# Performance work log

Hardware: AMD Instinct MI355X
Metric: run time of the kernel (lower is better)

The kernel has to match this reference:

```python
import jax, jax.numpy as jnp
import numpy as np

B, H, W, D = 4, 64, 64, 384
M, P = 12, 9
DH = D // M             # 32 head dim
DFF = 3 * D             # 1152 FFN hidden
N = H * W               # 4096 queries (single level)


def setup_inputs():
    key = jax.random.key(0)
    ks = jax.random.split(key, 12)
    g = lambda k, s, sc=0.02: jax.random.normal(k, s, jnp.float32) * sc
    return {
        "x": jax.random.normal(ks[0], (B, D, H, W), jnp.float32),
        "qry_masks": jnp.zeros((B, H, W), jnp.float32),
        "so_w": g(ks[1], (M * P * 2, D)), "so_b": g(ks[2], (M * P * 2,)),
        "aw_w": g(ks[3], (M * P, D)), "aw_b": g(ks[4], (M * P,)),
        "vp_w": g(ks[5], (D, D)), "vp_b": jnp.zeros((D,), jnp.float32),
        "op_w": g(ks[6], (D, D)), "op_b": jnp.zeros((D,), jnp.float32),
        "ln1_g": jnp.ones((D,), jnp.float32), "ln1_b": jnp.zeros((D,), jnp.float32),
        "w1": g(ks[7], (DFF, D)), "w2": g(ks[8], (D, DFF)),
        "ln2_g": jnp.ones((D,), jnp.float32), "ln2_b": jnp.zeros((D,), jnp.float32),
        "level_embed": g(ks[9], (1, D), 1.0),
    }


def _layernorm(x, g, b, eps=1e-5):
    mu = x.mean(-1, keepdims=True)
    v = ((x - mu) ** 2).mean(-1, keepdims=True)
    return (x - mu) * jax.lax.rsqrt(v + eps) * g + b


def _sine_pos(mask):
    # mask: [B,H,W] bool. mmdet SinePositionalEncoding(num_feats=D//2, normalize=True)
    not_mask = (~mask).astype(jnp.float32)
    y = jnp.cumsum(not_mask, 1)
    x = jnp.cumsum(not_mask, 2)
    eps, scale = 1e-6, 2.0 * np.pi
    y = y / (y[:, -1:, :] + eps) * scale
    x = x / (x[:, :, -1:] + eps) * scale
    nf = D // 2
    dim_t = 10000.0 ** (2.0 * (jnp.arange(nf) // 2).astype(jnp.float32) / nf)
    px, py = x[..., None] / dim_t, y[..., None] / dim_t

    def interleave(p):
        return jnp.stack([jnp.sin(p[..., 0::2]), jnp.cos(p[..., 1::2])], -1).reshape(p.shape[:-1] + (nf,))

    return jnp.concatenate([interleave(py), interleave(px)], -1)  # [B,H,W,D]


def _bilinear_gather(v, px, py):
    # v: [B,M,HW,DH]; px,py: [B,M,NP] pixel coords (grid_sample align_corners=False, zero pad)
    x0 = jnp.floor(px); y0 = jnp.floor(py)
    lx, ly = px - x0, py - y0
    x0i, y0i = x0.astype(jnp.int32), y0.astype(jnp.int32)
    out = jnp.zeros(v.shape[:2] + (px.shape[-1], v.shape[-1]), v.dtype)
    for dx, dy, wgt in ((0, 0, (1 - lx) * (1 - ly)), (1, 0, lx * (1 - ly)),
                        (0, 1, (1 - lx) * ly), (1, 1, lx * ly)):
        xi, yi = x0i + dx, y0i + dy
        valid = ((xi >= 0) & (xi < W) & (yi >= 0) & (yi < H)).astype(v.dtype)
        idx = jnp.clip(yi, 0, H - 1) * W + jnp.clip(xi, 0, W - 1)
        g = jnp.take_along_axis(v, idx[..., None], axis=2)  # [B,M,NP,DH]
        out = out + (wgt * valid)[..., None] * g
    return out


def _msdeform_attn(q, value_in, ref, mask_flat,
                   so_w, so_b, aw_w, aw_b, vp_w, vp_b, op_w, op_b):
    value = value_in @ vp_w.T + vp_b                      # [B,N,D]
    value = jnp.where(mask_flat[..., None], 0.0, value)
    so = (q @ so_w.T + so_b).reshape(B, N, M, P, 2)       # single level
    aw = jax.nn.softmax((q @ aw_w.T + aw_b).reshape(B, N, M, P), axis=-1)
    norm = jnp.array([W, H], jnp.float32)
    loc = ref[:, :, None, None, :] + so / norm            # [B,N,M,P,2] in [0,1]
    v = value.reshape(B, N, M, DH).transpose(0, 2, 1, 3)  # [B,M,HW,DH]
    px = (loc[..., 0] * W - 0.5).transpose(0, 2, 1, 3).reshape(B, M, N * P)
    py = (loc[..., 1] * H - 0.5).transpose(0, 2, 1, 3).reshape(B, M, N * P)
    sampled = _bilinear_gather(v, px, py).reshape(B, M, N, P, DH)
    out = jnp.einsum('bmnpd,bnmp->bnmd', sampled, aw).reshape(B, N, D)
    return out @ op_w.T + op_b


def reference(x, qry_masks, so_w, so_b, aw_w, aw_b, vp_w, vp_b, op_w, op_b,
              ln1_g, ln1_b, w1, w2, ln2_g, ln2_b, level_embed):
    mask = (qry_masks == 255.0)                           # [B,H,W] bool
    pos = _sine_pos(mask).reshape(B, N, D) + level_embed[0]
    src = x.reshape(B, D, N).transpose(0, 2, 1)           # [B,N,D]
    mask_flat = mask.reshape(B, N)
    gy, gx = jnp.meshgrid((jnp.arange(H, dtype=jnp.float32) + 0.5) / H,
                          (jnp.arange(W, dtype=jnp.float32) + 0.5) / W, indexing='ij')
    ref = jnp.stack([gx.reshape(-1), gy.reshape(-1)], -1)[None]  # [1,N,2] (x,y)
    q = src
    attn = _msdeform_attn(q + pos, q, ref, mask_flat,
                          so_w, so_b, aw_w, aw_b, vp_w, vp_b, op_w, op_b)
    q = _layernorm(q + attn, ln1_g, ln1_b)
    q = _layernorm(q + jax.nn.relu(q @ w1.T) @ w2.T, ln2_g, ln2_b)
    return q.transpose(0, 2, 1).reshape(B, D, H, W)
```

## Files before the change

kernel.cpp:

```cpp
#include <hip/hip_runtime.h>
#include <math.h>

#define Bc   4
#define Hc   64
#define Wc   64
#define Dc   384
#define Nc   4096
#define Mc   12
#define Pc   9
#define DHc  32
#define DFFc 1152
#define BNc  (Bc*Nc)

typedef __attribute__((ext_vector_type(8))) short short8;
typedef __attribute__((ext_vector_type(4))) float floatx4;

__device__ __forceinline__ ushort f2bf(float f) {
    union { float f; unsigned u; } v; v.f = f;
    unsigned r = v.u + 0x7fffu + ((v.u >> 16) & 1u);
    return (ushort)(r >> 16);
}
__device__ __forceinline__ float bf2f(ushort u) {
    union { unsigned u; float f; } v; v.u = (unsigned)u << 16; return v.f;
}

__device__ __forceinline__ void gload_lds16(const void* g, void* l) {
    __builtin_amdgcn_global_load_lds(
        (const __attribute__((address_space(1))) void*)(uintptr_t)g,
        (__attribute__((address_space(3))) void*)(uintptr_t)l,
        16, 0, 0);
}

#define SOW_N  82944
#define AWW_N  41472
#define VPW_N  147456
#define OPW_N  147456
#define W1_N   442368
#define W2_N   442368
#define WTOT   1304064

__global__ void init_kernel(const float* __restrict__ so_w,
                            const float* __restrict__ aw_w,
                            const float* __restrict__ vp_w,
                            const float* __restrict__ op_w,
                            const float* __restrict__ w1,
                            const float* __restrict__ w2,
                            const float* __restrict__ so_b,
                            const float* __restrict__ aw_b,
                            const float* __restrict__ qmask,
                            ushort* __restrict__ out,
                            float* __restrict__ bias_out,
                            float* __restrict__ cum_y,
                            float* __restrict__ cum_x) {
    int i = blockIdx.x * 256 + threadIdx.x;
    if (i < WTOT) {
        float v;
        int j = i;
        if (j < SOW_N) v = so_w[j];
        else if ((j -= SOW_N) < AWW_N) v = aw_w[j];
        else if ((j -= AWW_N) < VPW_N) v = vp_w[j];
        else if ((j -= VPW_N) < OPW_N) v = op_w[j];
        else if ((j -= OPW_N) < W1_N)  v = w1[j];
        else { j -= W1_N; v = w2[j]; }
        out[i] = f2bf(v);
        return;
    }
    int j = i - WTOT;
    if (j < 384) {
        bias_out[j] = (j < 216) ? so_b[j] : (j < 324 ? aw_b[j - 216] : 0.f);
        return;
    }
    int t = j - 384;
    if (t < Bc * Wc) {
        int b = t / Wc, w = t % Wc;
        float run = 0.f;
        for (int h = 0; h < Hc; ++h) {
            run += (qmask[(b * Hc + h) * Wc + w] == 255.0f) ? 0.f : 1.f;
            cum_y[(b * Hc + h) * Wc + w] = run;
        }
    } else if (t < Bc * Wc + Bc * Hc) {
        int t2 = t - Bc * Wc;
        int b = t2 / Hc, h = t2 % Hc;
        float run = 0.f;
        for (int w = 0; w < Wc; ++w) {
            run += (qmask[(b * Hc + h) * Wc + w] == 255.0f) ? 0.f : 1.f;
            cum_x[(b * Hc + h) * Wc + w] = run;
        }
    }
}

__global__ void transpose_pos_kernel(const float* __restrict__ x,
                                     const float* __restrict__ cum_y,
                                     const float* __restrict__ cum_x,
                                     const float* __restrict__ level_embed,
                                     ushort* __restrict__ src_bf,
                                     ushort* __restrict__ qpos_bf) {
    __shared__ float tile[32][33];
    int b  = blockIdx.z;
    int n0 = blockIdx.x * 32, d0 = blockIdx.y * 32;
    int tx = threadIdx.x, ty = threadIdx.y;
    tile[ty][tx] = x[((size_t)b * Dc + (d0 + ty)) * Nc + (n0 + tx)];
    __syncthreads();
    int n = n0 + ty, d = d0 + tx;
    float v = tile[tx][ty];
    size_t oi = ((size_t)b * Nc + n) * Dc + d;
    src_bf[oi] = f2bf(v);
    int h = n >> 6, w = n & 63;
    const float TWO_PI = 6.28318530717958647692f;
    float vy = cum_y[(b * Hc + h) * Wc + w] /
               (cum_y[(b * Hc + (Hc - 1)) * Wc + w] + 1e-6f) * TWO_PI;
    float vx = cum_x[(b * Hc + h) * Wc + w] /
               (cum_x[(b * Hc + h) * Wc + (Wc - 1)] + 1e-6f) * TWO_PI;
    int   i  = (d < 192) ? d : d - 192;
    float vv = (d < 192) ? vy : vx;
    float e   = (float)(i >> 1) * (2.0f / 192.0f);
    float idt = exp2f(e * -13.28771237954945f);
    float ang = vv * idt;
    float pe  = (i & 1) ? __cosf(ang) : __sinf(ang);
    qpos_bf[oi] = f2bf(v + pe + level_embed[d]);
}

template <int KT>
__device__ __forceinline__ void gemm_core(
        const ushort* __restrict__ A, const ushort* __restrict__ Wt,
        const float* __restrict__ bias,
        float* __restrict__ Cf, ushort* __restrict__ Cb,
        int Nout, int relu, const float* __restrict__ qmask,
        ushort* As, ushort* Bs) {
    constexpr int NCH = KT / 32;
    const int tid  = threadIdx.x;
    const int m0   = blockIdx.x * 128;
    const int n0   = blockIdx.y * 128;
    const int lane = tid & 63;
    const int wv   = tid >> 6;
    const int wr   = (wv >> 1) * 64;
    const int wc   = (wv & 1) * 64;
    const int quad = lane >> 4;
    const int lrow = lane & 15;
    const int srow = wv * 32 + (lane >> 2);
    const int scol = (lane & 3) * 8;

    floatx4 acc[4][4];
    #pragma unroll
    for (int i = 0; i < 4; ++i)
        #pragma unroll
        for (int j = 0; j < 4; ++j)
            acc[i][j] = (floatx4)(0.f);

    #pragma unroll
    for (int s = 0; s < 2; ++s) {
        gload_lds16(A  + (size_t)(m0 + srow + s * 16) * KT + scol,
                    As + wv * 1024 + s * 512);
        gload_lds16(Wt + (size_t)(n0 + srow + s * 16) * KT + scol,
                    Bs + wv * 1024 + s * 512);
    }

    for (int c = 0; c < NCH; ++c) {
        const int cur = c & 1;
        __syncthreads();
        if (c + 1 < NCH) {
            const int k0 = (c + 1) * 32;
            #pragma unroll
            for (int s = 0; s < 2; ++s) {
                gload_lds16(A  + (size_t)(m0 + srow + s * 16) * KT + k0 + scol,
                            As + (cur ^ 1) * 4096 + wv * 1024 + s * 512);
                gload_lds16(Wt + (size_t)(n0 + srow + s * 16) * KT + k0 + scol,
                            Bs + (cur ^ 1) * 4096 + wv * 1024 + s * 512);
            }
        }
        short8 afr[4], bfr[4];
        #pragma unroll
        for (int i = 0; i < 4; ++i)
            afr[i] = *(const short8*)(As + cur * 4096 +
                                      (wr + i * 16 + lrow) * 32 + quad * 8);
        #pragma unroll
        for (int j = 0; j < 4; ++j)
            bfr[j] = *(const short8*)(Bs + cur * 4096 +
                                      (wc + j * 16 + lrow) * 32 + quad * 8);
        #pragma unroll
        for (int i = 0; i < 4; ++i)
            #pragma unroll
            for (int j = 0; j < 4; ++j)
                acc[i][j] = __builtin_amdgcn_mfma_f32_16x16x32_bf16(
                    afr[i], bfr[j], acc[i][j], 0, 0, 0);
    }

    float mz[4][4];
    #pragma unroll
    for (int i = 0; i < 4; ++i)
        #pragma unroll
        for (int r = 0; r < 4; ++r) {
            int row = m0 + wr + i * 16 + quad * 4 + r;
            mz[i][r] = (qmask && qmask[row] == 255.0f) ? 0.f : 1.f;
        }

    #pragma unroll
    for (int i = 0; i < 4; ++i) {
        #pragma unroll
        for (int j = 0; j < 4; ++j) {
            int col = n0 + wc + j * 16 + lrow;
            if (col >= Nout) continue;
            float bsv = bias ? bias[col] : 0.f;
            #pragma unroll
            for (int r = 0; r < 4; ++r) {
                int row = m0 + wr + i * 16 + quad * 4 + r;
                float v = acc[i][j][r] + bsv;
                if (relu) v = fmaxf(v, 0.f);
                v *= mz[i][r];
                if (Cf) Cf[(size_t)row * Nout + col] = v;
                if (Cb) Cb[(size_t)row * Nout + col] = f2bf(v);
            }
        }
    }
}

template <int KT>
__global__ __launch_bounds__(256) void gemm_single_kernel(
        const ushort* __restrict__ A, const ushort* __restrict__ Wt,
        const float* __restrict__ bias,
        float* __restrict__ Cf, ushort* __restrict__ Cb,
        int Nout, int relu, const float* __restrict__ qmask) {
    __shared__ ushort As[2 * 128 * 32];
    __shared__ ushort Bs[2 * 128 * 32];
    gemm_core<KT>(A, Wt, bias, Cf, Cb, Nout, relu, qmask, As, Bs);
}

__global__ __launch_bounds__(256) void gemm_dual_kernel(
        const ushort* __restrict__ A0, const ushort* __restrict__ W0,
        const float* __restrict__ b0, float* __restrict__ Cf0,
        const ushort* __restrict__ A1, const ushort* __restrict__ W1,
        const float* __restrict__ b1, ushort* __restrict__ Cb1,
        const float* __restrict__ qmask) {
    __shared__ ushort As[2 * 128 * 32];
    __shared__ ushort Bs[2 * 128 * 32];
    if (blockIdx.z == 0)
        gemm_core<384>(A0, W0, b0, Cf0, nullptr, 384, 0, nullptr, As, Bs);
    else
        gemm_core<384>(A1, W1, b1, nullptr, Cb1, 384, 0, qmask, As, Bs);
}

__global__ __launch_bounds__(256) void deform_attn_kernel(
        const ushort* __restrict__ value_bf, const float* __restrict__ soaw,
        ushort* __restrict__ out) {
    int bid = blockIdx.x;
    int gb  = (bid & 7) * 384 + (bid >> 3);
    int gid = gb * 64 + (threadIdx.x >> 2);
    int l4  = threadIdx.x & 3;
    int m  = gid % Mc;
    int bn = gid / Mc;
    int b  = bn >> 12;
    int n  = bn & 4095;
    int h  = n >> 6, w = n & 63;
    const float* sop = soaw + (size_t)bn * 384 + m * 18;
    const float* lgt = soaw + (size_t)bn * 384 + 216 + m * Pc;
    float awv[Pc];
    float mx = lgt[0];
    #pragma unroll
    for (int i = 1; i < Pc; ++i) mx = fmaxf(mx, lgt[i]);
    float ssum = 0.f;
    #pragma unroll
    for (int i = 0; i < Pc; ++i) { awv[i] = __expf(lgt[i] - mx); ssum += awv[i]; }
    float sinv = 1.f / ssum;
    const ushort* vb = value_bf + ((size_t)b * Nc) * Dc + m * DHc + l4 * 8;
    float acc[8] = {0.f, 0.f, 0.f, 0.f, 0.f, 0.f, 0.f, 0.f};
    #pragma unroll
    for (int p = 0; p < Pc; ++p) {
        float2 so2 = *(const float2*)(sop + p * 2);
        float px = (float)w + so2.x;
        float py = (float)h + so2.y;
        float x0f = floorf(px), y0f = floorf(py);
        float lx = px - x0f, ly = py - y0f;
        int x0 = (int)x0f, y0 = (int)y0f;
        int x1 = x0 + 1,  y1 = y0 + 1;
        float a = awv[p] * sinv;
        float w00 = (1.f - lx) * (1.f - ly) * a;
        float w01 = lx * (1.f - ly) * a;
        float w10 = (1.f - lx) * ly * a;
        float w11 = lx * ly * a;
        bool bx0 = (unsigned)x0 < 64u, bx1 = (unsigned)x1 < 64u;
        bool by0 = (unsigned)y0 < 64u, by1 = (unsigned)y1 < 64u;
        w00 = (bx0 && by0) ? w00 : 0.f;
        w01 = (bx1 && by0) ? w01 : 0.f;
        w10 = (bx0 && by1) ? w10 : 0.f;
        w11 = (bx1 && by1) ? w11 : 0.f;
        int cx0 = min(max(x0, 0), 63), cx1 = min(max(x1, 0), 63);
        int cy0 = min(max(y0, 0), 63), cy1 = min(max(y1, 0), 63);
        uint4 q00 = *(const uint4*)(vb + (size_t)(cy0 * 64 + cx0) * Dc);
        uint4 q01 = *(const uint4*)(vb + (size_t)(cy0 * 64 + cx1) * Dc);
        uint4 q10 = *(const uint4*)(vb + (size_t)(cy1 * 64 + cx0) * Dc);
        uint4 q11 = *(const uint4*)(vb + (size_t)(cy1 * 64 + cx1) * Dc);
        union { unsigned u; float f; } t;
        #define ACC2(word, wg, k)                                   \
            t.u = (word) << 16;         acc[k]     += (wg) * t.f;   \
            t.u = (word) & 0xffff0000u; acc[k + 1] += (wg) * t.f;
        #define ACC8(q, wg) \
            ACC2((q).x, wg, 0) ACC2((q).y, wg, 2) ACC2((q).z, wg, 4) ACC2((q).w, wg, 6)
        ACC8(q00, w00) ACC8(q01, w01) ACC8(q10, w10) ACC8(q11, w11)
        #undef ACC8
        #undef ACC2
    }
    short8 o;
    #pragma unroll
    for (int k = 0; k < 8; ++k) o[k] = (short)f2bf(acc[k]);
    *(short8*)(out + (size_t)bn * Dc + m * DHc + l4 * 8) = o;
}

__global__ __launch_bounds__(128) void ln1_kernel(
        const ushort* __restrict__ a, const ushort* __restrict__ r,
        const float* __restrict__ g, const float* __restrict__ beta,
        float* __restrict__ outf, ushort* __restrict__ outb) {
    int row = blockIdx.x;
    int tid = threadIdx.x;
    float4 v = make_float4(0.f, 0.f, 0.f, 0.f);
    if (tid < 96) {
        ushort4 av = ((const ushort4*)(a + (size_t)row * Dc))[tid];
        ushort4 rv = ((const ushort4*)(r + (size_t)row * Dc))[tid];
        v.x = bf2f(av.x) + bf2f(rv.x); v.y = bf2f(av.y) + bf2f(rv.y);
        v.z = bf2f(av.z) + bf2f(rv.z); v.w = bf2f(av.w) + bf2f(rv.w);
    }
    float s1 = v.x + v.y + v.z + v.w;
    float s2 = v.x * v.x + v.y * v.y + v.z * v.z + v.w * v.w;
    __shared__ float sh1[128], sh2[128];
    sh1[tid] = s1; sh2[tid] = s2;
    __syncthreads();
    for (int off = 64; off > 0; off >>= 1) {
        if (tid < off) { sh1[tid] += sh1[tid + off]; sh2[tid] += sh2[tid + off]; }
        __syncthreads();
    }
    float mu  = sh1[0] * (1.0f / Dc);
    float var = sh2[0] * (1.0f / Dc) - mu * mu;
    float rs  = rsqrtf(var + 1e-5f);
    if (tid < 96) {
        float4 gv = ((const float4*)g)[tid];
        float4 bv = ((const float4*)beta)[tid];
        float4 o;
        o.x = (v.x - mu) * rs * gv.x + bv.x;
        o.y = (v.y - mu) * rs * gv.y + bv.y;
        o.z = (v.z - mu) * rs * gv.z + bv.z;
        o.w = (v.w - mu) * rs * gv.w + bv.w;
        ((float4*)(outf + (size_t)row * Dc))[tid] = o;
        ushort4 ob;
        ob.x = f2bf(o.x); ob.y = f2bf(o.y);
        ob.z = f2bf(o.z); ob.w = f2bf(o.w);
        ((ushort4*)(outb + (size_t)row * Dc))[tid] = ob;
    }
}

__global__ __launch_bounds__(256) void ln2_transpose_kernel(
        const float* __restrict__ q1, const ushort* __restrict__ r,
        const float* __restrict__ g, const float* __restrict__ beta,
        float* __restrict__ out) {
    __shared__ float tile[32 * 388];
    __shared__ float ps1[256], ps2[256];
    __shared__ float mu_[32], rs_[32];
    const int b  = blockIdx.y;
    const int n0 = blockIdx.x * 32;
    const int tid = threadIdx.x;
    const int rr  = tid >> 3;
    const int s8  = tid & 7;
    const size_t row = (size_t)b * Nc + n0 + rr;
    float s1 = 0.f, s2 = 0.f;
    #pragma unroll
    for (int i = 0; i < 12; ++i) {
        int c = s8 * 48 + i * 4;
        float4  av = *(const float4*)(q1 + row * Dc + c);
        ushort4 rv = *(const ushort4*)(r + row * Dc + c);
        float4 t;
        t.x = av.x + bf2f(rv.x); t.y = av.y + bf2f(rv.y);
        t.z = av.z + bf2f(rv.z); t.w = av.w + bf2f(rv.w);
        *(float4*)&tile[rr * 388 + c] = t;
        s1 += t.x + t.y + t.z + t.w;
        s2 += t.x * t.x + t.y * t.y + t.z * t.z + t.w * t.w;
    }
    ps1[tid] = s1; ps2[tid] = s2;
    __syncthreads();
    if (tid < 32) {
        float a1 = 0.f, a2 = 0.f;
        #pragma unroll
        for (int k = 0; k < 8; ++k) { a1 += ps1[tid * 8 + k]; a2 += ps2[tid * 8 + k]; }
        float mu = a1 * (1.0f / Dc);
        float var = a2 * (1.0f / Dc) - mu * mu;
        mu_[tid] = mu;
        rs_[tid] = rsqrtf(var + 1e-5f);
    }
    __syncthreads();
    const int dg = tid >> 5;
    const int nn = tid & 31;
    float mu = mu_[nn], rs = rs_[nn];
    #pragma unroll
    for (int j = 0; j < 48; ++j) {
        int d = dg * 48 + j;
        float val = (tile[nn * 388 + d] - mu) * rs * g[d] + beta[d];
        out[((size_t)b * Dc + d) * Nc + n0 + nn] = val;
    }
}

extern "C" void kernel_launch(void* const* d_in, const int* in_sizes, int n_in,
                              void* d_out, int out_size, void* d_ws, size_t ws_size,
                              hipStream_t stream) {
    (void)in_sizes; (void)n_in; (void)out_size; (void)ws_size;
    const float* x      = (const float*)d_in[0];
    const float* qmask  = (const float*)d_in[1];
    const float* so_w   = (const float*)d_in[2];
    const float* so_b   = (const float*)d_in[3];
    const float* aw_w   = (const float*)d_in[4];
    const float* aw_b   = (const float*)d_in[5];
    const float* vp_w   = (const float*)d_in[6];
    const float* vp_b   = (const float*)d_in[7];
    const float* op_w   = (const float*)d_in[8];
    const float* op_b   = (const float*)d_in[9];
    const float* ln1_g  = (const float*)d_in[10];
    const float* ln1_b  = (const float*)d_in[11];
    const float* w1     = (const float*)d_in[12];
    const float* w2     = (const float*)d_in[13];
    const float* ln2_g  = (const float*)d_in[14];
    const float* ln2_b  = (const float*)d_in[15];
    const float* lvl    = (const float*)d_in[16];
    float* out = (float*)d_out;

    float*  ws       = (float*)d_ws;
    float*  q1_f     = ws;
    ushort* src_bf   = (ushort*)(q1_f + 6291456);
    ushort* qpos_bf  = src_bf + 6291456;
    ushort* value_bf = qpos_bf + 6291456;
    ushort* proj_bf  = value_bf + 6291456;
    ushort* hbuf_bf  = proj_bf + 6291456;
    float*  soaw_f   = (float*)hbuf_bf;
    ushort* wbuf     = hbuf_bf + 18874368;
    float*  soaw_bias= (float*)(wbuf + 1304064);
    float*  cum_y    = soaw_bias + 384;
    float*  cum_x    = cum_y + 16384;

    const ushort* soaw_wb = wbuf;
    const ushort* vp_wb = soaw_wb + SOW_N + AWW_N;
    const ushort* op_wb = vp_wb + VPW_N;
    const ushort* w1_b  = op_wb + OPW_N;
    const ushort* w2_b  = w1_b + W1_N;

    init_kernel<<<(WTOT + 384 + 512 + 255) / 256, 256, 0, stream>>>(
        so_w, aw_w, vp_w, op_w, w1, w2, so_b, aw_b, qmask,
        wbuf, soaw_bias, cum_y, cum_x);
    transpose_pos_kernel<<<dim3(Nc / 32, Dc / 32, Bc), dim3(32, 32), 0, stream>>>(
        x, cum_y, cum_x, lvl, src_bf, qpos_bf);
    gemm_dual_kernel<<<dim3(BNc / 128, 3, 2), 256, 0, stream>>>(
        qpos_bf, soaw_wb, soaw_bias, soaw_f,
        src_bf, vp_wb, vp_b, value_bf, qmask);
    deform_attn_kernel<<<(BNc * Mc) / 64, 256, 0, stream>>>(
        value_bf, soaw_f, qpos_bf);
    gemm_single_kernel<384><<<dim3(BNc / 128, 3), 256, 0, stream>>>(
        qpos_bf, op_wb, op_b, nullptr, proj_bf, Dc, 0, nullptr);
    ln1_kernel<<<BNc, 128, 0, stream>>>(
        src_bf, proj_bf, ln1_g, ln1_b, q1_f, qpos_bf);
    gemm_single_kernel<384><<<dim3(BNc / 128, 9), 256, 0, stream>>>(
        qpos_bf, w1_b, nullptr, nullptr, hbuf_bf, DFFc, 1, nullptr);
    gemm_single_kernel<1152><<<dim3(BNc / 128, 3), 256, 0, stream>>>(
        hbuf_bf, w2_b, nullptr, nullptr, proj_bf, Dc, 0, nullptr);
    ln2_transpose_kernel<<<dim3(Nc / 32, Bc), 256, 0, stream>>>(
        q1_f, proj_bf, ln2_g, ln2_b, out);
}
```

Measured before the change: 271.9 us.

## Fuse residual-add and LayerNorm into full-row GEMM epilogues

Adds a GEMM kernel where each block computes a full 64x384 output row tile. The epilogue adds the residual, computes the LayerNorm statistics with shuffles and shared memory, and writes the normalised result. For the FFN2 path it also transposes through shared memory into the final NCHW layout. This replaces the output-projection GEMM plus ln1 and the FFN2 GEMM plus the ln2-transpose kernel. It removes the proj_bf round trip through memory and two launches, at the cost of large 512-thread blocks with about 256 blocks in total, which lowers occupancy and parallelism per GEMM.

```diff
diff --git a/kernel.cpp b/kernel.cpp
--- a/kernel.cpp
+++ b/kernel.cpp
@@ -237,6 +237,187 @@
         gemm_core<384>(A0, W0, b0, Cf0, nullptr, 384, 0, nullptr, As, Bs);
     else
         gemm_core<384>(A1, W1, b1, nullptr, Cb1, 384, 0, qmask, As, Bs);
+}
+
+template <int KT, int MODE>
+__global__ __launch_bounds__(512) void gemm_fullrow_kernel(
+        const ushort* __restrict__ A, const ushort* __restrict__ Wt,
+        const float* __restrict__ bias, const void* __restrict__ resid,
+        const float* __restrict__ g, const float* __restrict__ beta,
+        float* __restrict__ outf, ushort* __restrict__ outb) {
+    constexpr int NCH = KT / 32;
+    __shared__ ushort smem[28672];
+    __shared__ float eps1[8][64], eps2[8][64];
+    __shared__ float mu_l[64], rs_l[64];
+    ushort* As = smem;
+    ushort* Bs = smem + 4096;
+    const int tid  = threadIdx.x;
+    const int lane = tid & 63;
+    const int wv   = tid >> 6;
+    const int quad = lane >> 4;
+    const int lrow = lane & 15;
+    const int m0   = blockIdx.x * 64;
+    const int srow = lane >> 2;
+    const int scol = (lane & 3) * 8;
+
+    floatx4 acc[4][3];
+    #pragma unroll
+    for (int i = 0; i < 4; ++i)
+        #pragma unroll
+        for (int j = 0; j < 3; ++j)
+            acc[i][j] = (floatx4)(0.f);
+
+    if (wv < 4)
+        gload_lds16(A + (size_t)(m0 + wv * 16 + srow) * KT + scol,
+                    As + wv * 512);
+    #pragma unroll
+    for (int s = 0; s < 3; ++s)
+        gload_lds16(Wt + (size_t)(wv * 48 + s * 16 + srow) * KT + scol,
+                    Bs + wv * 1536 + s * 512);
+
+    for (int c = 0; c < NCH; ++c) {
+        const int cur = c & 1;
+        __syncthreads();
+        if (c + 1 < NCH) {
+            const int k0 = (c + 1) * 32;
+            if (wv < 4)
+                gload_lds16(A + (size_t)(m0 + wv * 16 + srow) * KT + k0 + scol,
+                            As + (cur ^ 1) * 2048 + wv * 512);
+            #pragma unroll
+            for (int s = 0; s < 3; ++s)
+                gload_lds16(Wt + (size_t)(wv * 48 + s * 16 + srow) * KT + k0 + scol,
+                            Bs + (cur ^ 1) * 12288 + wv * 1536 + s * 512);
+        }
+        short8 afr[4], bfr[3];
+        #pragma unroll
+        for (int i = 0; i < 4; ++i)
+            afr[i] = *(const short8*)(As + cur * 2048 +
+                                      (i * 16 + lrow) * 32 + quad * 8);
+        #pragma unroll
+        for (int j = 0; j < 3; ++j)
+            bfr[j] = *(const short8*)(Bs + cur * 12288 +
+                                      (wv * 48 + j * 16 + lrow) * 32 + quad * 8);
+        #pragma unroll
+        for (int i = 0; i < 4; ++i)
+            #pragma unroll
+            for (int j = 0; j < 3; ++j)
+                acc[i][j] = __builtin_amdgcn_mfma_f32_16x16x32_bf16(
+                    afr[i], bfr[j], acc[i][j], 0, 0, 0);
+    }
+
+    float s1[16], s2[16];
+    #pragma unroll
+    for (int k = 0; k < 16; ++k) { s1[k] = 0.f; s2[k] = 0.f; }
+    #pragma unroll
+    for (int i = 0; i < 4; ++i) {
+        #pragma unroll
+        for (int r = 0; r < 4; ++r) {
+            int rl = i * 16 + quad * 4 + r;
+            #pragma unroll
+            for (int j = 0; j < 3; ++j) {
+                int col = wv * 48 + j * 16 + lrow;
+                float t = acc[i][j][r];
+                if (bias) t += bias[col];
+                if (MODE == 0)
+                    t += bf2f(((const ushort*)resid)[(size_t)(m0 + rl) * Dc + col]);
+                else
+                    t += ((const float*)resid)[(size_t)(m0 + rl) * Dc + col];
+                acc[i][j][r] = t;
+                s1[i * 4 + r] += t;
+                s2[i * 4 + r] += t * t;
+            }
+        }
+    }
+    #pragma unroll
+    for (int m = 1; m < 16; m <<= 1) {
+        #pragma unroll
+        for (int k = 0; k < 16; ++k) {
+            s1[k] += __shfl_xor(s1[k], m);
+            s2[k] += __shfl_xor(s2[k], m);
+        }
+    }
+    if (lrow == 0) {
+        #pragma unroll
+        for (int i = 0; i < 4; ++i)
+            #pragma unroll
+            for (int r = 0; r < 4; ++r) {
+                int rl = i * 16 + quad * 4 + r;
+                eps1[wv][rl] = s1[i * 4 + r];
+                eps2[wv][rl] = s2[i * 4 + r];
+            }
+    }
+    __syncthreads();
+    if (tid < 64) {
+        float a1 = 0.f, a2 = 0.f;
+        #pragma unroll
+        for (int w = 0; w < 8; ++w) { a1 += eps1[w][tid]; a2 += eps2[w][tid]; }
+        float mu  = a1 * (1.0f / Dc);
+        float var = a2 * (1.0f / Dc) - mu * mu;
+        mu_l[tid] = mu;
+        rs_l[tid] = rsqrtf(var + 1e-5f);
+    }
+    __syncthreads();
+
+    #pragma unroll
+    for (int i = 0; i < 4; ++i) {
+        #pragma unroll
+        for (int r = 0; r < 4; ++r) {
+            int rl = i * 16 + quad * 4 + r;
+            float mu = mu_l[rl], rs = rs_l[rl];
+            #pragma unroll
+            for (int j = 0; j < 3; ++j) {
+                int col = wv * 48 + j * 16 + lrow;
+                acc[i][j][r] = (acc[i][j][r] - mu) * rs * g[col] + beta[col];
+            }
+        }
+    }
+
+    if (MODE == 0) {
+        #pragma unroll
+        for (int i = 0; i < 4; ++i)
+            #pragma unroll
+            for (int j = 0; j < 3; ++j) {
+                int col = wv * 48 + j * 16 + lrow;
+                #pragma unroll
+                for (int r = 0; r < 4; ++r) {
+                    int rl = i * 16 + quad * 4 + r;
+                    float v = acc[i][j][r];
+                    outf[(size_t)(m0 + rl) * Dc + col] = v;
+                    outb[(size_t)(m0 + rl) * Dc + col] = f2bf(v);
+                }
+            }
+    } else {
+        float* tile = (float*)smem;
+        const int b   = m0 >> 12;
+        const int n0r = m0 & 4095;
+        #pragma unroll
+        for (int gp = 0; gp < 2; ++gp) {
+            __syncthreads();
+            if ((wv >> 2) == gp) {
+                int cbase = (wv & 3) * 48;
+                #pragma unroll
+                for (int i = 0; i < 4; ++i)
+                    #pragma unroll
+                    for (int j = 0; j < 3; ++j) {
+                        int c = cbase + j * 16 + lrow;
+                        #pragma unroll
+                        for (int r = 0; r < 4; ++r) {
+                            int rl = i * 16 + quad * 4 + r;
+                            tile[rl * 193 + c] = acc[i][j][r];
+                        }
+                    }
+            }
+            __syncthreads();
+            const int row = tid & 63;
+            const int cp  = tid >> 6;
+            #pragma unroll
+            for (int it = 0; it < 24; ++it) {
+                int c = it * 8 + cp;
+                outf[((size_t)(b * Dc + gp * 192 + c)) * Nc + n0r + row] =
+                    tile[row * 193 + c];
+            }
+        }
+    }
 }
 
 __global__ __launch_bounds__(256) void deform_attn_kernel(
@@ -305,96 +486,6 @@
     *(short8*)(out + (size_t)bn * Dc + m * DHc + l4 * 8) = o;
 }
 
-__global__ __launch_bounds__(128) void ln1_kernel(
-        const ushort* __restrict__ a, const ushort* __restrict__ r,
-        const float* __restrict__ g, const float* __restrict__ beta,
-        float* __restrict__ outf, ushort* __restrict__ outb) {
-    int row = blockIdx.x;
-    int tid = threadIdx.x;
-    float4 v = make_float4(0.f, 0.f, 0.f, 0.f);
-    if (tid < 96) {
-        ushort4 av = ((const ushort4*)(a + (size_t)row * Dc))[tid];
-        ushort4 rv = ((const ushort4*)(r + (size_t)row * Dc))[tid];
-        v.x = bf2f(av.x) + bf2f(rv.x); v.y = bf2f(av.y) + bf2f(rv.y);
-        v.z = bf2f(av.z) + bf2f(rv.z); v.w = bf2f(av.w) + bf2f(rv.w);
-    }
-    float s1 = v.x + v.y + v.z + v.w;
-    float s2 = v.x * v.x + v.y * v.y + v.z * v.z + v.w * v.w;
-    __shared__ float sh1[128], sh2[128];
-    sh1[tid] = s1; sh2[tid] = s2;
-    __syncthreads();
-    for (int off = 64; off > 0; off >>= 1) {
-        if (tid < off) { sh1[tid] += sh1[tid + off]; sh2[tid] += sh2[tid + off]; }
-        __syncthreads();
-    }
-    float mu  = sh1[0] * (1.0f / Dc);
-    float var = sh2[0] * (1.0f / Dc) - mu * mu;
-    float rs  = rsqrtf(var + 1e-5f);
-    if (tid < 96) {
-        float4 gv = ((const float4*)g)[tid];
-        float4 bv = ((const float4*)beta)[tid];
-        float4 o;
-        o.x = (v.x - mu) * rs * gv.x + bv.x;
-        o.y = (v.y - mu) * rs * gv.y + bv.y;
-        o.z = (v.z - mu) * rs * gv.z + bv.z;
-        o.w = (v.w - mu) * rs * gv.w + bv.w;
-        ((float4*)(outf + (size_t)row * Dc))[tid] = o;
-        ushort4 ob;
-        ob.x = f2bf(o.x); ob.y = f2bf(o.y);
-        ob.z = f2bf(o.z); ob.w = f2bf(o.w);
-        ((ushort4*)(outb + (size_t)row * Dc))[tid] = ob;
-    }
-}
-
-__global__ __launch_bounds__(256) void ln2_transpose_kernel(
-        const float* __restrict__ q1, const ushort* __restrict__ r,
-        const float* __restrict__ g, const float* __restrict__ beta,
-        float* __restrict__ out) {
-    __shared__ float tile[32 * 388];
-    __shared__ float ps1[256], ps2[256];
-    __shared__ float mu_[32], rs_[32];
-    const int b  = blockIdx.y;
-    const int n0 = blockIdx.x * 32;
-    const int tid = threadIdx.x;
-    const int rr  = tid >> 3;
-    const int s8  = tid & 7;
-    const size_t row = (size_t)b * Nc + n0 + rr;
-    float s1 = 0.f, s2 = 0.f;
-    #pragma unroll
-    for (int i = 0; i < 12; ++i) {
-        int c = s8 * 48 + i * 4;
-        float4  av = *(const float4*)(q1 + row * Dc + c);
-        ushort4 rv = *(const ushort4*)(r + row * Dc + c);
-        float4 t;
-        t.x = av.x + bf2f(rv.x); t.y = av.y + bf2f(rv.y);
-        t.z = av.z + bf2f(rv.z); t.w = av.w + bf2f(rv.w);
-        *(float4*)&tile[rr * 388 + c] = t;
-        s1 += t.x + t.y + t.z + t.w;
-        s2 += t.x * t.x + t.y * t.y + t.z * t.z + t.w * t.w;
-    }
-    ps1[tid] = s1; ps2[tid] = s2;
-    __syncthreads();
-    if (tid < 32) {
-        float a1 = 0.f, a2 = 0.f;
-        #pragma unroll
-        for (int k = 0; k < 8; ++k) { a1 += ps1[tid * 8 + k]; a2 += ps2[tid * 8 + k]; }
-        float mu = a1 * (1.0f / Dc);
-        float var = a2 * (1.0f / Dc) - mu * mu;
-        mu_[tid] = mu;
-        rs_[tid] = rsqrtf(var + 1e-5f);
-    }
-    __syncthreads();
-    const int dg = tid >> 5;
-    const int nn = tid & 31;
-    float mu = mu_[nn], rs = rs_[nn];
-    #pragma unroll
-    for (int j = 0; j < 48; ++j) {
-        int d = dg * 48 + j;
-        float val = (tile[nn * 388 + d] - mu) * rs * g[d] + beta[d];
-        out[((size_t)b * Dc + d) * Nc + n0 + nn] = val;
-    }
-}
-
 extern "C" void kernel_launch(void* const* d_in, const int* in_sizes, int n_in,
                               void* d_out, int out_size, void* d_ws, size_t ws_size,
                               hipStream_t stream) {
@@ -423,8 +514,7 @@
     ushort* src_bf   = (ushort*)(q1_f + 6291456);
     ushort* qpos_bf  = src_bf + 6291456;
     ushort* value_bf = qpos_bf + 6291456;
-    ushort* proj_bf  = value_bf + 6291456;
-    ushort* hbuf_bf  = proj_bf + 6291456;
+    ushort* hbuf_bf  = value_bf + 6291456;
     float*  soaw_f   = (float*)hbuf_bf;
     ushort* wbuf     = hbuf_bf + 18874368;
     float*  soaw_bias= (float*)(wbuf + 1304064);
@@ -447,14 +537,10 @@
         src_bf, vp_wb, vp_b, value_bf, qmask);
     deform_attn_kernel<<<(BNc * Mc) / 64, 256, 0, stream>>>(
         value_bf, soaw_f, qpos_bf);
-    gemm_single_kernel<384><<<dim3(BNc / 128, 3), 256, 0, stream>>>(
-        qpos_bf, op_wb, op_b, nullptr, proj_bf, Dc, 0, nullptr);
-    ln1_kernel<<<BNc, 128, 0, stream>>>(
-        src_bf, proj_bf, ln1_g, ln1_b, q1_f, qpos_bf);
+    gemm_fullrow_kernel<384, 0><<<BNc / 64, 512, 0, stream>>>(
+        qpos_bf, op_wb, op_b, src_bf, ln1_g, ln1_b, q1_f, qpos_bf);
     gemm_single_kernel<384><<<dim3(BNc / 128, 9), 256, 0, stream>>>(
         qpos_bf, w1_b, nullptr, nullptr, hbuf_bf, DFFc, 1, nullptr);
-    gemm_single_kernel<1152><<<dim3(BNc / 128, 3), 256, 0, stream>>>(
-        hbuf_bf, w2_b, nullptr, nullptr, proj_bf, Dc, 0, nullptr);
-    ln2_transpose_kernel<<<dim3(Nc / 32, Bc), 256, 0, stream>>>(
-        q1_f, proj_bf, ln2_g, ln2_b, out);
-}
+    gemm_fullrow_kernel<1152, 1><<<BNc / 64, 512, 0, stream>>>(
+        hbuf_bf, w2_b, nullptr, q1_f, ln2_g, ln2_b, out, nullptr);
+}
```

Measured after the change: 265.2 us. -2.5%, faster.
